# Performance work log

Hardware: AMD Instinct MI355X
Metric: run time of the kernel (lower is better)

Reference implementation:

```python
import jax, jax.numpy as jnp
import numpy as np
from jax import lax

B = 2048
C = 8
H = W = 14
NP = H * W  # 196
DIM = 192
THETA = 0.7


def _unfold3(z):
    # z: [B, C, H, W] -> patches [B, C, 9, H, W], matching F.unfold(kernel=3, pad=1)
    p = jnp.pad(z, ((0, 0), (0, 0), (1, 1), (1, 1)))
    return jnp.stack([p[:, :, dy:dy + H, dx:dx + W]
                      for dy in range(3) for dx in range(3)], axis=2)


def setup_inputs() -> dict:
    key = jax.random.key(0)
    ks = jax.random.split(key, 10)
    s = 0.1
    return {
        "x": jax.random.normal(ks[0], (B, 1 + NP, DIM), dtype=jnp.float32),
        "W1": jax.random.normal(ks[1], (C, DIM), dtype=jnp.float32) * s,      # linear1 192->8
        "b1": jax.random.normal(ks[2], (C,), dtype=jnp.float32) * s,
        "conv1_w": jax.random.normal(ks[3], (C, C), dtype=jnp.float32) * s,   # 1x1 conv
        "conv1_b": jax.random.normal(ks[4], (C,), dtype=jnp.float32) * s,
        "cdc_w": jax.random.normal(ks[5], (C, C, 1, 5), dtype=jnp.float32) * s,
        "wc1": jax.random.normal(ks[6], (C, C), dtype=jnp.float32) * s,       # WConv1 (1x1)
        "wc2": jax.random.normal(ks[7], (C, C), dtype=jnp.float32) * s,       # WConv2 (1x1)
        "hist_w": jax.random.normal(ks[8], (DIM, C), dtype=jnp.float32) * s,  # linear 8->192
        "hist_b": jax.random.normal(ks[9], (DIM,), dtype=jnp.float32) * s,
    }


def reference(x, W1, b1, conv1_w, conv1_b, cdc_w, wc1, wc2, hist_w, hist_b):
    class_token, tok = x[:, :1, :], x[:, 1:, :]
    # linear1: [B,196,192] -> [B,196,8]
    t = jnp.einsum('bnd,cd->bnc', tok, W1) + b1
    # -> [B,8,14,14]
    t = t.reshape(-1, H, W, C).transpose(0, 3, 1, 2)

    # conv1 (1x1)
    x1 = jnp.einsum('bihw,oi->bohw', t, conv1_w) + conv1_b[None, :, None, None]

    # CDC: scatter the 1x5 weights into a 3x3 cross-shaped kernel
    w5 = cdc_w[:, :, 0, :]  # [O,I,5]
    z = jnp.zeros((C, C, 1), dtype=cdc_w.dtype)
    k9 = jnp.concatenate([z, w5[:, :, 0:1], z,
                          w5[:, :, 1:2], w5[:, :, 2:3], w5[:, :, 3:4],
                          z, w5[:, :, 4:5], z], axis=2).reshape(C, C, 3, 3)
    out_normal = lax.conv_general_dilated(
        t, k9, window_strides=(1, 1), padding=((1, 1), (1, 1)),
        dimension_numbers=('NCHW', 'OIHW', 'NCHW'))
    kernel_diff = cdc_w.sum(axis=(2, 3))  # [O,I]
    out_diff = jnp.einsum('bihw,oi->bohw', t, kernel_diff)
    x2 = out_normal - THETA * out_diff

    z_star = x1 + x2  # [B,8,14,14]

    # TokenHistogram
    mu = jnp.einsum('bihw,oi->bohw', z_star, wc1)
    gamma = jnp.einsum('bihw,oi->bohw', z_star, wc2)
    zp = _unfold3(z_star)   # [B,8,9,14,14]
    mp = _unfold3(mu)
    gp = _unfold3(gamma)
    u = gp * (zp - mp)
    z_hist = jnp.exp(-u * u).sum(axis=2) / 9.0  # [B,8,14,14]
    # torch .reshape(-1, NP, 8): plain row-major reshape (mixes C and HW)
    z_hist = z_hist.reshape(-1, NP, C)
    y = jnp.einsum('bnc,dc->bnd', z_hist, hist_w) + hist_b  # [B,196,192]

    return jnp.concatenate([class_token, y], axis=1)
```

## Files before the change

kernel.cpp:

```cpp
#include <hip/hip_runtime.h>


#define DIMD 192
#define IMGS 37824
#define NIMG 2048

typedef __fp16 half2_t __attribute__((ext_vector_type(2)));

__device__ __forceinline__ half2_t u2h(unsigned u) {
    union { unsigned u; half2_t h; } cv; cv.u = u; return cv.h;
}
__device__ __forceinline__ unsigned h2u(half2_t h) {
    union { half2_t h; unsigned u; } cv; cv.h = h; return cv.u;
}

__global__ void k0_pack(const float* __restrict__ W1,
                        const float* __restrict__ hist_w,
                        unsigned* __restrict__ wsA,
                        unsigned* __restrict__ wsD)
{
    int f = threadIdx.x + blockIdx.x * 256;
    if (f < 768) {
        wsA[f] = h2u(__builtin_amdgcn_cvt_pkrtz(W1[2*f], W1[2*f+1]));
        wsD[f] = h2u(__builtin_amdgcn_cvt_pkrtz(hist_w[2*f], hist_w[2*f+1]));
    }
}

__launch_bounds__(256)
__global__ void sadapter_kernel(
    const float* __restrict__ x,
    const float* __restrict__ b1,
    const float* __restrict__ conv1_w,
    const float* __restrict__ conv1_b,
    const float* __restrict__ cdc_w,
    const float* __restrict__ wc1,
    const float* __restrict__ wc2,
    const unsigned* __restrict__ wsA,
    const unsigned* __restrict__ wsD,
    const float* __restrict__ hist_b,
    float* __restrict__ out)
{
    __shared__ float smem[4608];
    float* TS  = smem;
    float* ZH  = smem;
    float* PS  = smem + 2048;
    float* WB2 = smem + 4096;

    const int tid = threadIdx.x;
    const float* xb   = x   + (size_t)blockIdx.x * IMGS;
    float*       outb = out + (size_t)blockIdx.x * IMGS;

    {
        float4 z4 = make_float4(0.f, 0.f, 0.f, 0.f);
        float4 o4 = make_float4(1.f, 1.f, 1.f, 1.f);
        ((float4*)TS)[tid]       = z4;
        ((float4*)TS)[tid + 256] = z4;
        ((float4*)PS)[tid]       = o4;
        ((float4*)PS)[tid + 256] = o4;
    }
    if (tid < 64) {
        const float* c5 = cdc_w + tid * 5;
        float k0 = c5[0], k1 = c5[1], k2 = c5[2], k3 = c5[3], k4 = c5[4];
        float kd = k0 + k1 + k2 + k3 + k4;
        float* wp = WB2 + tid * 8;
        wp[0] = conv1_w[tid] + k2 - 0.7f * kd;
        wp[1] = k0; wp[2] = k1; wp[3] = k3; wp[4] = k4;
        wp[5] = wc1[tid];
        wp[6] = wc2[tid];
        wp[7] = 0.f;
    }
    __syncthreads();

    if (tid < 196) {
        const float4* rowp = (const float4*)(xb + DIMD + tid * DIMD);
        float acc[8];
        #pragma unroll
        for (int c = 0; c < 8; ++c) acc[c] = b1[c];
        #pragma unroll
        for (int blk = 0; blk < 6; ++blk) {
            float4 tv[8];
            #pragma unroll
            for (int u = 0; u < 8; ++u) tv[u] = rowp[blk * 8 + u];
            half2_t tp16[16];
            #pragma unroll
            for (int u = 0; u < 8; ++u) {
                tp16[2*u]   = __builtin_amdgcn_cvt_pkrtz(tv[u].x, tv[u].y);
                tp16[2*u+1] = __builtin_amdgcn_cvt_pkrtz(tv[u].z, tv[u].w);
            }
            #pragma unroll
            for (int c = 0; c < 8; ++c) {
                const unsigned* wp = wsA + c * 96 + blk * 16;
                #pragma unroll
                for (int j = 0; j < 16; ++j)
                    acc[c] = __builtin_amdgcn_fdot2(tp16[j], u2h(wp[j]), acc[c], false);
            }
        }
        int h = tid / 14, w = tid - h * 14;
        float* tp = TS + (h + 1) * 16 + (w + 1);
        #pragma unroll
        for (int c = 0; c < 8; ++c) tp[c * 256] = acc[c];
    } else if (tid >= 208) {
        ((float4*)outb)[tid - 208] = ((const float4*)xb)[tid - 208];
    }
    __syncthreads();

    if (tid < 196) {
        int h = tid / 14, w = tid - h * 14;
        const float* tp = TS + (h + 1) * 16 + (w + 1);
        float zv[8];
        #pragma unroll
        for (int c = 0; c < 8; ++c) zv[c] = conv1_b[c];
        #pragma unroll
        for (int i = 0; i < 8; ++i) {
            float t0 = tp[i * 256];
            float tu = tp[i * 256 - 16];
            float td = tp[i * 256 + 16];
            float tl = tp[i * 256 - 1];
            float tr = tp[i * 256 + 1];
            #pragma unroll
            for (int c = 0; c < 8; ++c) {
                const float* wp = WB2 + (c * 8 + i) * 8;
                float4 wv = *(const float4*)wp;
                float wd = wp[4];
                zv[c] += wv.x * t0 + wv.y * tu + wv.z * tl + wv.w * tr + wd * td;
            }
        }
        float* pp = PS + (h + 1) * 16 + (w + 1);
        #pragma unroll
        for (int c = 0; c < 8; ++c) {
            float mu = 0.f, ga = 0.f;
            #pragma unroll
            for (int i = 0; i < 8; ++i) {
                const float* wp = WB2 + (c * 8 + i) * 8;
                mu += wp[5] * zv[i];
                ga += wp[6] * zv[i];
            }
            float e = ga * (zv[c] - mu);
            pp[c * 256] = __expf(-e * e);
        }
    }
    __syncthreads();

    const int l  = tid & 63;
    const int wv = tid >> 6;
    const uint4 wa = *(const uint4*)(wsD + l * 4);
    const uint4 wb = *(const uint4*)(wsD + (l + 64) * 4);
    const uint4 wc = *(const uint4*)(wsD + (l + 128) * 4);
    const float ba  = hist_b[l];
    const float bb  = hist_b[l + 64];
    const float bc_ = hist_b[l + 128];

    if (tid < 196) {
        int h = tid / 14, w = tid - h * 14;
        const float* pb = PS + h * 16 + w;
        #pragma unroll
        for (int c = 0; c < 8; ++c) {
            const float* pr = pb + c * 256;
            float s9 = pr[0]  + pr[1]  + pr[2]
                     + pr[16] + pr[17] + pr[18]
                     + pr[32] + pr[33] + pr[34];
            ZH[c * 196 + tid] = s9 * (1.f / 9.f);
        }
    }
    __syncthreads();

    {
        float* oy = outb + DIMD;
        const int n2beg = wv * 49;
        #pragma unroll 2
        for (int k = 0; k < 49; ++k) {
            const int n2 = n2beg + k;
            const float4 z0 = *(const float4*)(ZH + n2 * 8);
            const float4 z1 = *(const float4*)(ZH + n2 * 8 + 4);
            half2_t zp0 = __builtin_amdgcn_cvt_pkrtz(z0.x, z0.y);
            half2_t zp1 = __builtin_amdgcn_cvt_pkrtz(z0.z, z0.w);
            half2_t zp2 = __builtin_amdgcn_cvt_pkrtz(z1.x, z1.y);
            half2_t zp3 = __builtin_amdgcn_cvt_pkrtz(z1.z, z1.w);
            float a0 = ba, a1 = bb, a2 = bc_;
            a0 = __builtin_amdgcn_fdot2(zp0, u2h(wa.x), a0, false);
            a0 = __builtin_amdgcn_fdot2(zp1, u2h(wa.y), a0, false);
            a0 = __builtin_amdgcn_fdot2(zp2, u2h(wa.z), a0, false);
            a0 = __builtin_amdgcn_fdot2(zp3, u2h(wa.w), a0, false);
            a1 = __builtin_amdgcn_fdot2(zp0, u2h(wb.x), a1, false);
            a1 = __builtin_amdgcn_fdot2(zp1, u2h(wb.y), a1, false);
            a1 = __builtin_amdgcn_fdot2(zp2, u2h(wb.z), a1, false);
            a1 = __builtin_amdgcn_fdot2(zp3, u2h(wb.w), a1, false);
            a2 = __builtin_amdgcn_fdot2(zp0, u2h(wc.x), a2, false);
            a2 = __builtin_amdgcn_fdot2(zp1, u2h(wc.y), a2, false);
            a2 = __builtin_amdgcn_fdot2(zp2, u2h(wc.z), a2, false);
            a2 = __builtin_amdgcn_fdot2(zp3, u2h(wc.w), a2, false);
            float* orow = oy + n2 * DIMD;
            orow[l]       = a0;
            orow[l + 64]  = a1;
            orow[l + 128] = a2;
        }
    }
}

__launch_bounds__(256)
__global__ void sadapter_fused(
    const float* __restrict__ x,
    const float* __restrict__ W1,
    const float* __restrict__ b1,
    const float* __restrict__ conv1_w,
    const float* __restrict__ conv1_b,
    const float* __restrict__ cdc_w,
    const float* __restrict__ wc1,
    const float* __restrict__ wc2,
    const float* __restrict__ hist_w,
    const float* __restrict__ hist_b,
    float* __restrict__ out)
{
    __shared__ float smem[4608];
    float* TS  = smem;
    float* ZH  = smem;
    float* PS  = smem + 2048;
    float* WB2 = smem + 4096;
    const int tid = threadIdx.x;
    const float* xb   = x   + (size_t)blockIdx.x * IMGS;
    float*       outb = out + (size_t)blockIdx.x * IMGS;

    {
        float4 z4 = make_float4(0.f,0.f,0.f,0.f), o4 = make_float4(1.f,1.f,1.f,1.f);
        ((float4*)TS)[tid] = z4; ((float4*)TS)[tid+256] = z4;
        ((float4*)PS)[tid] = o4; ((float4*)PS)[tid+256] = o4;
    }
    if (tid < 64) {
        const float* c5 = cdc_w + tid * 5;
        float k0=c5[0],k1=c5[1],k2=c5[2],k3=c5[3],k4=c5[4];
        float kd = k0+k1+k2+k3+k4;
        float* wp = WB2 + tid*8;
        wp[0]=conv1_w[tid]+k2-0.7f*kd; wp[1]=k0; wp[2]=k1; wp[3]=k3; wp[4]=k4;
        wp[5]=wc1[tid]; wp[6]=wc2[tid]; wp[7]=0.f;
    }
    __syncthreads();
    if (tid < 196) {
        const float4* rowp = (const float4*)(xb + DIMD + tid * DIMD);
        float acc[8];
        #pragma unroll
        for (int c=0;c<8;++c) acc[c]=b1[c];
        #pragma unroll
        for (int blk=0; blk<6; ++blk) {
            float4 tv[8];
            #pragma unroll
            for (int u=0;u<8;++u) tv[u]=rowp[blk*8+u];
            #pragma unroll
            for (int c=0;c<8;++c) {
                const float* wrow = W1 + c*DIMD + blk*32;
                #pragma unroll
                for (int u=0;u<8;++u)
                    acc[c] += tv[u].x*wrow[u*4+0]+tv[u].y*wrow[u*4+1]
                            + tv[u].z*wrow[u*4+2]+tv[u].w*wrow[u*4+3];
            }
        }
        int h=tid/14, w=tid-h*14;
        float* tp = TS + (h+1)*16 + (w+1);
        #pragma unroll
        for (int c=0;c<8;++c) tp[c*256]=acc[c];
    } else if (tid >= 208) {
        ((float4*)outb)[tid-208] = ((const float4*)xb)[tid-208];
    }
    __syncthreads();
    if (tid < 196) {
        int h=tid/14, w=tid-h*14;
        const float* tp = TS + (h+1)*16 + (w+1);
        float zv[8];
        #pragma unroll
        for (int c=0;c<8;++c) zv[c]=conv1_b[c];
        #pragma unroll
        for (int i=0;i<8;++i) {
            float t0=tp[i*256], tu=tp[i*256-16], td=tp[i*256+16], tl=tp[i*256-1], tr=tp[i*256+1];
            #pragma unroll
            for (int c=0;c<8;++c) {
                const float* wp = WB2 + (c*8+i)*8;
                float4 wv = *(const float4*)wp;
                zv[c] += wv.x*t0 + wv.y*tu + wv.z*tl + wv.w*tr + wp[4]*td;
            }
        }
        float* pp = PS + (h+1)*16 + (w+1);
        #pragma unroll
        for (int c=0;c<8;++c) {
            float mu=0.f, ga=0.f;
            #pragma unroll
            for (int i=0;i<8;++i) {
                const float* wp = WB2 + (c*8+i)*8;
                mu += wp[5]*zv[i]; ga += wp[6]*zv[i];
            }
            float e = ga*(zv[c]-mu);
            pp[c*256] = __expf(-e*e);
        }
    }
    __syncthreads();
    const int l  = tid & 63;
    const int wv = tid >> 6;
    const float4 ha0 = *(const float4*)(hist_w + l * 8);
    const float4 ha1 = *(const float4*)(hist_w + l * 8 + 4);
    const float4 hb0 = *(const float4*)(hist_w + (l + 64) * 8);
    const float4 hb1 = *(const float4*)(hist_w + (l + 64) * 8 + 4);
    const float4 hc0 = *(const float4*)(hist_w + (l + 128) * 8);
    const float4 hc1 = *(const float4*)(hist_w + (l + 128) * 8 + 4);
    const float  ba  = hist_b[l];
    const float  bb  = hist_b[l + 64];
    const float  bc_ = hist_b[l + 128];
    if (tid < 196) {
        int h=tid/14, w=tid-h*14;
        const float* pb = PS + h*16 + w;
        #pragma unroll
        for (int c=0;c<8;++c) {
            const float* pr = pb + c*256;
            float s9 = pr[0]+pr[1]+pr[2]+pr[16]+pr[17]+pr[18]+pr[32]+pr[33]+pr[34];
            ZH[c*196+tid] = s9*(1.f/9.f);
        }
    }
    __syncthreads();
    {
        float* oy = outb + DIMD;
        const int n2beg = wv * 49;
        #pragma unroll 2
        for (int k = 0; k < 49; ++k) {
            const int n2 = n2beg + k;
            const float4 z0 = *(const float4*)(ZH + n2 * 8);
            const float4 z1 = *(const float4*)(ZH + n2 * 8 + 4);
            float a0 = ba + z0.x*ha0.x + z0.y*ha0.y + z0.z*ha0.z + z0.w*ha0.w
                          + z1.x*ha1.x + z1.y*ha1.y + z1.z*ha1.z + z1.w*ha1.w;
            float a1 = bb + z0.x*hb0.x + z0.y*hb0.y + z0.z*hb0.z + z0.w*hb0.w
                          + z1.x*hb1.x + z1.y*hb1.y + z1.z*hb1.z + z1.w*hb1.w;
            float a2 = bc_+ z0.x*hc0.x + z0.y*hc0.y + z0.z*hc0.z + z0.w*hc0.w
                          + z1.x*hc1.x + z1.y*hc1.y + z1.z*hc1.z + z1.w*hc1.w;
            float* orow = oy + n2 * DIMD;
            orow[l]       = a0;
            orow[l + 64]  = a1;
            orow[l + 128] = a2;
        }
    }
}

extern "C" void kernel_launch(void* const* d_in, const int* in_sizes, int n_in,
                              void* d_out, int out_size, void* d_ws, size_t ws_size,
                              hipStream_t stream)
{
    const float* x       = (const float*)d_in[0];
    const float* W1      = (const float*)d_in[1];
    const float* b1      = (const float*)d_in[2];
    const float* conv1_w = (const float*)d_in[3];
    const float* conv1_b = (const float*)d_in[4];
    const float* cdc_w   = (const float*)d_in[5];
    const float* wc1     = (const float*)d_in[6];
    const float* wc2     = (const float*)d_in[7];
    const float* hist_w  = (const float*)d_in[8];
    const float* hist_b  = (const float*)d_in[9];
    float* out = (float*)d_out;

    const size_t need = 2 * 768 * sizeof(unsigned);
    if (ws_size >= need) {
        unsigned* wsA = (unsigned*)d_ws;
        unsigned* wsD = wsA + 768;
        k0_pack<<<3, 256, 0, stream>>>(W1, hist_w, wsA, wsD);
        sadapter_kernel<<<NIMG, 256, 0, stream>>>(
            x, b1, conv1_w, conv1_b, cdc_w, wc1, wc2, wsA, wsD, hist_b, out);
    } else {
        sadapter_fused<<<NIMG, 256, 0, stream>>>(
            x, W1, b1, conv1_w, conv1_b, cdc_w, wc1, wc2, hist_w, hist_b, out);
    }
}
```

Before: 152.8 us.

## Process two images per block, overlapping output GEMM with next image's linear1

The kernel now launches half as many blocks, and each block handles two images. While two waves write image 0's output projection, the other two waves compute image 1's linear1 loads and dot products into the second shared buffer. The aim is to overlap the global-store-heavy output phase with the global-load-heavy input phase. In exchange, only half the threads work on each of those phases, there are more barriers, and the grid holds fewer blocks to hide latency.

```diff
diff --git a/kernel.cpp b/kernel.cpp
--- a/kernel.cpp
+++ b/kernel.cpp
@@ -4,6 +4,7 @@
 #define DIMD 192
 #define IMGS 37824
 #define NIMG 2048
+#define HB   1024
 
 typedef __fp16 half2_t __attribute__((ext_vector_type(2)));
 
@@ -26,8 +27,68 @@
     }
 }
 
+__device__ __forceinline__ void phase_bc(const float* __restrict__ TSrc,
+                                         float* __restrict__ Pdst,
+                                         const float* __restrict__ WB2,
+                                         const float* __restrict__ conv1_b,
+                                         int tid)
+{
+    if (tid < 196) {
+        int h = tid / 14, w = tid - h * 14;
+        const float* tp = TSrc + (h + 1) * 16 + (w + 1);
+        float zv[8];
+        #pragma unroll
+        for (int c = 0; c < 8; ++c) zv[c] = conv1_b[c];
+        #pragma unroll
+        for (int i = 0; i < 8; ++i) {
+            float t0 = tp[i * 256];
+            float tu = tp[i * 256 - 16];
+            float td = tp[i * 256 + 16];
+            float tl = tp[i * 256 - 1];
+            float tr = tp[i * 256 + 1];
+            #pragma unroll
+            for (int c = 0; c < 8; ++c) {
+                const float* wp = WB2 + (c * 8 + i) * 8;
+                float4 wv = *(const float4*)wp;
+                float wd = wp[4];
+                zv[c] += wv.x * t0 + wv.y * tu + wv.z * tl + wv.w * tr + wd * td;
+            }
+        }
+        float* pp = Pdst + (h + 1) * 16 + (w + 1);
+        #pragma unroll
+        for (int c = 0; c < 8; ++c) {
+            float mu = 0.f, ga = 0.f;
+            #pragma unroll
+            for (int i = 0; i < 8; ++i) {
+                const float* wp = WB2 + (c * 8 + i) * 8;
+                mu += wp[5] * zv[i];
+                ga += wp[6] * zv[i];
+            }
+            float e = ga * (zv[c] - mu);
+            pp[c * 256] = __expf(-e * e);
+        }
+    }
+}
+
+__device__ __forceinline__ void phase_c2(const float* __restrict__ Psrc,
+                                         float* __restrict__ ZHdst, int tid)
+{
+    if (tid < 196) {
+        int h = tid / 14, w = tid - h * 14;
+        const float* pb = Psrc + h * 16 + w;
+        #pragma unroll
+        for (int c = 0; c < 8; ++c) {
+            const float* pr = pb + c * 256;
+            float s9 = pr[0]  + pr[1]  + pr[2]
+                     + pr[16] + pr[17] + pr[18]
+                     + pr[32] + pr[33] + pr[34];
+            ZHdst[c * 196 + tid] = s9 * (1.f / 9.f);
+        }
+    }
+}
+
 __launch_bounds__(256)
-__global__ void sadapter_kernel(
+__global__ void sadapter_pipe(
     const float* __restrict__ x,
     const float* __restrict__ b1,
     const float* __restrict__ conv1_w,
@@ -41,23 +102,25 @@
     float* __restrict__ out)
 {
     __shared__ float smem[4608];
-    float* TS  = smem;
-    float* ZH  = smem;
-    float* PS  = smem + 2048;
+    float* r1  = smem;
+    float* r2  = smem + 2048;
     float* WB2 = smem + 4096;
 
     const int tid = threadIdx.x;
-    const float* xb   = x   + (size_t)blockIdx.x * IMGS;
-    float*       outb = out + (size_t)blockIdx.x * IMGS;
-
-    {
-        float4 z4 = make_float4(0.f, 0.f, 0.f, 0.f);
-        float4 o4 = make_float4(1.f, 1.f, 1.f, 1.f);
-        ((float4*)TS)[tid]       = z4;
-        ((float4*)TS)[tid + 256] = z4;
-        ((float4*)PS)[tid]       = o4;
-        ((float4*)PS)[tid + 256] = o4;
-    }
+    const int l   = tid & 63;
+    const int wv  = tid >> 6;
+    const float* xb0 = x   + (size_t)blockIdx.x * IMGS;
+    const float* xb1 = xb0 + (size_t)HB * IMGS;
+    float* ob0 = out + (size_t)blockIdx.x * IMGS;
+    float* ob1 = ob0 + (size_t)HB * IMGS;
+
+    const float4 z4 = make_float4(0.f, 0.f, 0.f, 0.f);
+    const float4 o4 = make_float4(1.f, 1.f, 1.f, 1.f);
+
+    ((float4*)r1)[tid]       = z4;
+    ((float4*)r1)[tid + 256] = z4;
+    ((float4*)r2)[tid]       = o4;
+    ((float4*)r2)[tid + 256] = o4;
     if (tid < 64) {
         const float* c5 = cdc_w + tid * 5;
         float k0 = c5[0], k1 = c5[1], k2 = c5[2], k3 = c5[3], k4 = c5[4];
@@ -72,7 +135,7 @@
     __syncthreads();
 
     if (tid < 196) {
-        const float4* rowp = (const float4*)(xb + DIMD + tid * DIMD);
+        const float4* rowp = (const float4*)(xb0 + DIMD + tid * DIMD);
         float acc[8];
         #pragma unroll
         for (int c = 0; c < 8; ++c) acc[c] = b1[c];
@@ -96,86 +159,45 @@
             }
         }
         int h = tid / 14, w = tid - h * 14;
-        float* tp = TS + (h + 1) * 16 + (w + 1);
+        float* tp = r1 + (h + 1) * 16 + (w + 1);
         #pragma unroll
         for (int c = 0; c < 8; ++c) tp[c * 256] = acc[c];
-    } else if (tid >= 208) {
-        ((float4*)outb)[tid - 208] = ((const float4*)xb)[tid - 208];
-    }
-    __syncthreads();
-
-    if (tid < 196) {
-        int h = tid / 14, w = tid - h * 14;
-        const float* tp = TS + (h + 1) * 16 + (w + 1);
-        float zv[8];
-        #pragma unroll
-        for (int c = 0; c < 8; ++c) zv[c] = conv1_b[c];
-        #pragma unroll
-        for (int i = 0; i < 8; ++i) {
-            float t0 = tp[i * 256];
-            float tu = tp[i * 256 - 16];
-            float td = tp[i * 256 + 16];
-            float tl = tp[i * 256 - 1];
-            float tr = tp[i * 256 + 1];
-            #pragma unroll
-            for (int c = 0; c < 8; ++c) {
-                const float* wp = WB2 + (c * 8 + i) * 8;
-                float4 wv = *(const float4*)wp;
-                float wd = wp[4];
-                zv[c] += wv.x * t0 + wv.y * tu + wv.z * tl + wv.w * tr + wd * td;
-            }
-        }
-        float* pp = PS + (h + 1) * 16 + (w + 1);
-        #pragma unroll
-        for (int c = 0; c < 8; ++c) {
-            float mu = 0.f, ga = 0.f;
-            #pragma unroll
-            for (int i = 0; i < 8; ++i) {
-                const float* wp = WB2 + (c * 8 + i) * 8;
-                mu += wp[5] * zv[i];
-                ga += wp[6] * zv[i];
-            }
-            float e = ga * (zv[c] - mu);
-            pp[c * 256] = __expf(-e * e);
-        }
-    }
-    __syncthreads();
-
-    const int l  = tid & 63;
-    const int wv = tid >> 6;
-    const uint4 wa = *(const uint4*)(wsD + l * 4);
-    const uint4 wb = *(const uint4*)(wsD + (l + 64) * 4);
-    const uint4 wc = *(const uint4*)(wsD + (l + 128) * 4);
-    const float ba  = hist_b[l];
-    const float bb  = hist_b[l + 64];
-    const float bc_ = hist_b[l + 128];
-
-    if (tid < 196) {
-        int h = tid / 14, w = tid - h * 14;
-        const float* pb = PS + h * 16 + w;
-        #pragma unroll
-        for (int c = 0; c < 8; ++c) {
-            const float* pr = pb + c * 256;
-            float s9 = pr[0]  + pr[1]  + pr[2]
-                     + pr[16] + pr[17] + pr[18]
-                     + pr[32] + pr[33] + pr[34];
-            ZH[c * 196 + tid] = s9 * (1.f / 9.f);
-        }
-    }
-    __syncthreads();
-
-    {
-        float* oy = outb + DIMD;
-        const int n2beg = wv * 49;
+    } else {
+        for (int f = tid - 196; f < 96; f += 60) {
+            int img = f / 48, j = f - img * 48;
+            ((float4*)(img ? ob1 : ob0))[j] = ((const float4*)(img ? xb1 : xb0))[j];
+        }
+    }
+    __syncthreads();
+
+    phase_bc(r1, r2, WB2, conv1_b, tid);
+    __syncthreads();
+
+    phase_c2(r2, r1, tid);
+    __syncthreads();
+
+    ((float4*)r2)[tid]       = z4;
+    ((float4*)r2)[tid + 256] = z4;
+    __syncthreads();
+
+    if (wv < 2) {
+        const uint4 wa = *(const uint4*)(wsD + l * 4);
+        const uint4 wb = *(const uint4*)(wsD + (l + 64) * 4);
+        const uint4 wc = *(const uint4*)(wsD + (l + 128) * 4);
+        const float ba  = hist_b[l];
+        const float bb  = hist_b[l + 64];
+        const float bc_ = hist_b[l + 128];
+        float* oy = ob0 + DIMD;
+        const int n2beg = wv * 98;
         #pragma unroll 2
-        for (int k = 0; k < 49; ++k) {
+        for (int k = 0; k < 98; ++k) {
             const int n2 = n2beg + k;
-            const float4 z0 = *(const float4*)(ZH + n2 * 8);
-            const float4 z1 = *(const float4*)(ZH + n2 * 8 + 4);
-            half2_t zp0 = __builtin_amdgcn_cvt_pkrtz(z0.x, z0.y);
-            half2_t zp1 = __builtin_amdgcn_cvt_pkrtz(z0.z, z0.w);
-            half2_t zp2 = __builtin_amdgcn_cvt_pkrtz(z1.x, z1.y);
-            half2_t zp3 = __builtin_amdgcn_cvt_pkrtz(z1.z, z1.w);
+            const float4 zz0 = *(const float4*)(r1 + n2 * 8);
+            const float4 zz1 = *(const float4*)(r1 + n2 * 8 + 4);
+            half2_t zp0 = __builtin_amdgcn_cvt_pkrtz(zz0.x, zz0.y);
+            half2_t zp1 = __builtin_amdgcn_cvt_pkrtz(zz0.z, zz0.w);
+            half2_t zp2 = __builtin_amdgcn_cvt_pkrtz(zz1.x, zz1.y);
+            half2_t zp3 = __builtin_amdgcn_cvt_pkrtz(zz1.z, zz1.w);
             float a0 = ba, a1 = bb, a2 = bc_;
             a0 = __builtin_amdgcn_fdot2(zp0, u2h(wa.x), a0, false);
             a0 = __builtin_amdgcn_fdot2(zp1, u2h(wa.y), a0, false);
@@ -194,6 +216,90 @@
             orow[l + 64]  = a1;
             orow[l + 128] = a2;
         }
+    } else {
+        const int local = tid - 128;
+        #pragma unroll
+        for (int pass = 0; pass < 2; ++pass) {
+            const int n = local + pass * 128;
+            if (n < 196) {
+                const float4* rowp = (const float4*)(xb1 + DIMD + n * DIMD);
+                float acc[8];
+                #pragma unroll
+                for (int c = 0; c < 8; ++c) acc[c] = b1[c];
+                #pragma unroll
+                for (int blk = 0; blk < 12; ++blk) {
+                    float4 tv[4];
+                    #pragma unroll
+                    for (int u = 0; u < 4; ++u) tv[u] = rowp[blk * 4 + u];
+                    half2_t tp16[8];
+                    #pragma unroll
+                    for (int u = 0; u < 4; ++u) {
+                        tp16[2*u]   = __builtin_amdgcn_cvt_pkrtz(tv[u].x, tv[u].y);
+                        tp16[2*u+1] = __builtin_amdgcn_cvt_pkrtz(tv[u].z, tv[u].w);
+                    }
+                    #pragma unroll
+                    for (int c = 0; c < 8; ++c) {
+                        const unsigned* wp = wsA + c * 96 + blk * 8;
+                        #pragma unroll
+                        for (int j = 0; j < 8; ++j)
+                            acc[c] = __builtin_amdgcn_fdot2(tp16[j], u2h(wp[j]), acc[c], false);
+                    }
+                }
+                int h = n / 14, w = n - h * 14;
+                float* tp = r2 + (h + 1) * 16 + (w + 1);
+                #pragma unroll
+                for (int c = 0; c < 8; ++c) tp[c * 256] = acc[c];
+            }
+        }
+    }
+    __syncthreads();
+
+    ((float4*)r1)[tid]       = o4;
+    ((float4*)r1)[tid + 256] = o4;
+    __syncthreads();
+
+    phase_bc(r2, r1, WB2, conv1_b, tid);
+    __syncthreads();
+
+    phase_c2(r1, r2, tid);
+    __syncthreads();
+
+    {
+        const uint4 wa = *(const uint4*)(wsD + l * 4);
+        const uint4 wb = *(const uint4*)(wsD + (l + 64) * 4);
+        const uint4 wc = *(const uint4*)(wsD + (l + 128) * 4);
+        const float ba  = hist_b[l];
+        const float bb  = hist_b[l + 64];
+        const float bc_ = hist_b[l + 128];
+        float* oy = ob1 + DIMD;
+        const int n2beg = wv * 49;
+        #pragma unroll 2
+        for (int k = 0; k < 49; ++k) {
+            const int n2 = n2beg + k;
+            const float4 zz0 = *(const float4*)(r2 + n2 * 8);
+            const float4 zz1 = *(const float4*)(r2 + n2 * 8 + 4);
+            half2_t zp0 = __builtin_amdgcn_cvt_pkrtz(zz0.x, zz0.y);
+            half2_t zp1 = __builtin_amdgcn_cvt_pkrtz(zz0.z, zz0.w);
+            half2_t zp2 = __builtin_amdgcn_cvt_pkrtz(zz1.x, zz1.y);
+            half2_t zp3 = __builtin_amdgcn_cvt_pkrtz(zz1.z, zz1.w);
+            float a0 = ba, a1 = bb, a2 = bc_;
+            a0 = __builtin_amdgcn_fdot2(zp0, u2h(wa.x), a0, false);
+            a0 = __builtin_amdgcn_fdot2(zp1, u2h(wa.y), a0, false);
+            a0 = __builtin_amdgcn_fdot2(zp2, u2h(wa.z), a0, false);
+            a0 = __builtin_amdgcn_fdot2(zp3, u2h(wa.w), a0, false);
+            a1 = __builtin_amdgcn_fdot2(zp0, u2h(wb.x), a1, false);
+            a1 = __builtin_amdgcn_fdot2(zp1, u2h(wb.y), a1, false);
+            a1 = __builtin_amdgcn_fdot2(zp2, u2h(wb.z), a1, false);
+            a1 = __builtin_amdgcn_fdot2(zp3, u2h(wb.w), a1, false);
+            a2 = __builtin_amdgcn_fdot2(zp0, u2h(wc.x), a2, false);
+            a2 = __builtin_amdgcn_fdot2(zp1, u2h(wc.y), a2, false);
+            a2 = __builtin_amdgcn_fdot2(zp2, u2h(wc.z), a2, false);
+            a2 = __builtin_amdgcn_fdot2(zp3, u2h(wc.w), a2, false);
+            float* orow = oy + n2 * DIMD;
+            orow[l]       = a0;
+            orow[l + 64]  = a1;
+            orow[l + 128] = a2;
+        }
     }
 }
 
@@ -261,35 +367,7 @@
         ((float4*)outb)[tid-208] = ((const float4*)xb)[tid-208];
     }
     __syncthreads();
-    if (tid < 196) {
-        int h=tid/14, w=tid-h*14;
-        const float* tp = TS + (h+1)*16 + (w+1);
-        float zv[8];
-        #pragma unroll
-        for (int c=0;c<8;++c) zv[c]=conv1_b[c];
-        #pragma unroll
-        for (int i=0;i<8;++i) {
-            float t0=tp[i*256], tu=tp[i*256-16], td=tp[i*256+16], tl=tp[i*256-1], tr=tp[i*256+1];
-            #pragma unroll
-            for (int c=0;c<8;++c) {
-                const float* wp = WB2 + (c*8+i)*8;
-                float4 wv = *(const float4*)wp;
-                zv[c] += wv.x*t0 + wv.y*tu + wv.z*tl + wv.w*tr + wp[4]*td;
-            }
-        }
-        float* pp = PS + (h+1)*16 + (w+1);
-        #pragma unroll
-        for (int c=0;c<8;++c) {
-            float mu=0.f, ga=0.f;
-            #pragma unroll
-            for (int i=0;i<8;++i) {
-                const float* wp = WB2 + (c*8+i)*8;
-                mu += wp[5]*zv[i]; ga += wp[6]*zv[i];
-            }
-            float e = ga*(zv[c]-mu);
-            pp[c*256] = __expf(-e*e);
-        }
-    }
+    phase_bc(TS, PS, WB2, conv1_b, tid);
     __syncthreads();
     const int l  = tid & 63;
     const int wv = tid >> 6;
@@ -302,16 +380,7 @@
     const float  ba  = hist_b[l];
     const float  bb  = hist_b[l + 64];
     const float  bc_ = hist_b[l + 128];
-    if (tid < 196) {
-        int h=tid/14, w=tid-h*14;
-        const float* pb = PS + h*16 + w;
-        #pragma unroll
-        for (int c=0;c<8;++c) {
-            const float* pr = pb + c*256;
-            float s9 = pr[0]+pr[1]+pr[2]+pr[16]+pr[17]+pr[18]+pr[32]+pr[33]+pr[34];
-            ZH[c*196+tid] = s9*(1.f/9.f);
-        }
-    }
+    phase_c2(PS, ZH, tid);
     __syncthreads();
     {
         float* oy = outb + DIMD;
@@ -356,7 +425,7 @@
         unsigned* wsA = (unsigned*)d_ws;
         unsigned* wsD = wsA + 768;
         k0_pack<<<3, 256, 0, stream>>>(W1, hist_w, wsA, wsD);
-        sadapter_kernel<<<NIMG, 256, 0, stream>>>(
+        sadapter_pipe<<<HB, 256, 0, stream>>>(
             x, b1, conv1_w, conv1_b, cdc_w, wc1, wc2, wsA, wsD, hist_b, out);
     } else {
         sadapter_fused<<<NIMG, 256, 0, stream>>>(
```

Result: slower. 157.8 us (+3.3%).
